# Kernel tuning notes

Hardware: AMD Instinct MI355X
Metric: run time of the kernel (lower is better)

## Reference

```python
import jax, jax.numpy as jnp
import numpy as np

INPUT_DIMS = 32
OUTPUT_DIMS = 1024
SEQ_LEN = 1024
BATCH = 64


def positional_encoding(max_len, d_model):
    pos = np.arange(max_len)[:, None].astype(np.float64)      # [L,1]
    i = np.arange(d_model)[None, :].astype(np.float64)        # [1,D]
    even_i = i - (i % 2)                                      # i for even, i-1 for odd
    angle = pos / np.power(10000.0, even_i / d_model)         # [L,D]
    pe = np.where(i % 2 == 0, np.sin(angle), np.cos(angle))
    return jnp.asarray(pe, dtype=jnp.float32)


def activation_quant(x):
    # per-token absmax int8 quant (BitNet b1.58)
    scale = 127.0 / jnp.clip(jnp.max(jnp.abs(x), axis=-1, keepdims=True), 1e-5, None)
    return jnp.clip(jnp.round(x * scale), -128, 127) / scale


def weight_quant(w):
    # per-tensor ternary quant via mean absmax
    scale = 1.0 / jnp.clip(jnp.mean(jnp.abs(w)), 1e-5, None)
    return jnp.clip(jnp.round(w * scale), -1, 1) / scale


def setup_inputs() -> dict:
    key = jax.random.key(0)
    k1, k2, k3 = jax.random.split(key, 3)
    x = jax.random.normal(k1, (BATCH, SEQ_LEN, INPUT_DIMS), dtype=jnp.float32)
    bound = 1.0 / np.sqrt(INPUT_DIMS)
    W = jax.random.uniform(k2, (OUTPUT_DIMS, INPUT_DIMS), minval=-bound, maxval=bound, dtype=jnp.float32)
    b = jax.random.uniform(k3, (OUTPUT_DIMS,), minval=-bound, maxval=bound, dtype=jnp.float32)
    return {"x": x, "W": W, "b": b}


def reference(x, W, b):
    # BitLinear with straight-through estimator
    x_eff = x + jax.lax.stop_gradient(activation_quant(x) - x)
    w_eff = W + jax.lax.stop_gradient(weight_quant(W) - W)
    emb = jnp.einsum('bsk,ok->bso', x_eff, w_eff) + b  # [B,S,O]
    pe = positional_encoding(SEQ_LEN, OUTPUT_DIMS)     # [L,O]
    return emb + pe[: emb.shape[-2]]
```

## Files before the change

### kernel.cpp

```cpp
#include <hip/hip_runtime.h>
#include <cstdint>
#include <cstddef>

#define BATCH   64
#define SEQLEN  1024
#define KDIM    32
#define ODIM    1024
#define NTOK    (BATCH * SEQLEN)

#define NWP 8
#define NQX 8192
#define NPE 1024

typedef __attribute__((ext_vector_type(8))) short bf16x8;
typedef __attribute__((ext_vector_type(4))) float f32x4;

__device__ __forceinline__ unsigned short f32_to_bf16_exact(float f) {
    union { float f; unsigned int u; } cv; cv.f = f;
    return (unsigned short)(cv.u >> 16);
}

__global__ __launch_bounds__(256) void prep_kernel(const float* __restrict__ x,
                                                   const float* __restrict__ W,
                                                   const float* __restrict__ bias,
                                                   float* __restrict__ partial,
                                                   unsigned short* __restrict__ xq,
                                                   float* __restrict__ rxs,
                                                   float* __restrict__ add) {
    const int blk = blockIdx.x;
    const int t   = threadIdx.x;

    if (blk < NWP) {
        __shared__ float red[256];
        const float4* W4 = reinterpret_cast<const float4*>(W) + (size_t)blk * 1024 + t * 4;
        float acc = 0.f;
        #pragma unroll
        for (int j = 0; j < 4; ++j) {
            float4 v = W4[j];
            acc += fabsf(v.x) + fabsf(v.y) + fabsf(v.z) + fabsf(v.w);
        }
        red[t] = acc;
        __syncthreads();
        for (int step = 128; step > 0; step >>= 1) {
            if (t < step) red[t] += red[t + step];
            __syncthreads();
        }
        if (t == 0) partial[blk] = red[0];
    } else if (blk < NWP + NQX) {
        const int idx = (blk - NWP) * 256 + t;
        float v = x[idx];
        float a = fabsf(v);
        #pragma unroll
        for (int off = 1; off < 32; off <<= 1)
            a = fmaxf(a, __shfl_xor(a, off, 32));
        float am = fmaxf(a, 1e-5f);
        float scale = 127.0f / am;
        xq[idx] = f32_to_bf16_exact(rintf(v * scale));
        if ((idx & 31) == 0) rxs[idx >> 5] = am * (1.0f / 127.0f);
    } else {
        const int g  = (blk - NWP - NQX) * 256 + t;
        const int oe = (g << 2) & (ODIM - 1);
        const int s  = g >> 8;
        const float C = -0.012976281620653759f;
        const float sf = (float)s;
        float a0 = sf * exp2f(C * (float)oe);
        float a1 = sf * exp2f(C * (float)(oe + 2));
        f32x4 bv = *reinterpret_cast<const f32x4*>(bias + oe);
        f32x4 r;
        r[0] = bv[0] + sinf(a0);
        r[1] = bv[1] + cosf(a0);
        r[2] = bv[2] + sinf(a1);
        r[3] = bv[3] + cosf(a1);
        *reinterpret_cast<f32x4*>(add + ((size_t)g << 2)) = r;
    }
}

__global__ __launch_bounds__(256) void bitgemm(
    const unsigned short* __restrict__ xq,
    const float*          __restrict__ rxs,
    const float*          __restrict__ W,
    const float*          __restrict__ partial,
    const float*          __restrict__ add,
    float* __restrict__ out)
{
    const int lane = threadIdx.x & 63;
    const int wid  = threadIdx.x >> 6;
    const int l15  = lane & 15;
    const int hi   = lane >> 4;

    const int lb   = (blockIdx.x & 7) * 256 + (blockIdx.x >> 3);
    const int oblk = lb & 31;
    const int sblk = lb >> 5;
    const int o0   = oblk * 32;
    const int s0   = sblk * 16;

    float tot = 0.f;
    #pragma unroll
    for (int p = 0; p < 8; ++p) tot += partial[p];
    const float rw = fmaxf(tot * (1.0f / 32768.0f), 1e-5f);
    const float sc = 1.0f / rw;

    bf16x8 afrag[2];
    #pragma unroll
    for (int f = 0; f < 2; ++f) {
        const float* wr = W + (size_t)(o0 + f * 16 + l15) * KDIM + hi * 8;
        float4 wa = *reinterpret_cast<const float4*>(wr);
        float4 wb = *reinterpret_cast<const float4*>(wr + 4);
        float e[8] = {wa.x, wa.y, wa.z, wa.w, wb.x, wb.y, wb.z, wb.w};
        union { bf16x8 v; unsigned short s[8]; } u;
        #pragma unroll
        for (int j = 0; j < 8; ++j)
            u.s[j] = f32_to_bf16_exact(fminf(fmaxf(rintf(e[j] * sc), -1.0f), 1.0f));
        afrag[f] = u.v;
    }

    f32x4 addf[2];
    #pragma unroll
    for (int f = 0; f < 2; ++f)
        addf[f] = *reinterpret_cast<const f32x4*>(
            add + (size_t)(s0 + l15) * ODIM + o0 + f * 16 + hi * 4);

    #pragma unroll 4
    for (int i = 0; i < 16; ++i) {
        const int b   = wid * 16 + i;
        const int tok = (b << 10) + s0 + l15;

        bf16x8 bfrag = *reinterpret_cast<const bf16x8*>(
            xq + ((size_t)tok << 5) + hi * 8);
        const float rxw = rxs[tok] * rw;

        float* op = out + ((size_t)tok << 10) + o0 + hi * 4;
        #pragma unroll
        for (int f = 0; f < 2; ++f) {
            f32x4 acc = (f32x4){0.f, 0.f, 0.f, 0.f};
            acc = __builtin_amdgcn_mfma_f32_16x16x32_bf16(afrag[f], bfrag, acc, 0, 0, 0);
            f32x4 r;
            #pragma unroll
            for (int j = 0; j < 4; ++j)
                r[j] = fmaf(acc[j], rxw, addf[f][j]);
            *reinterpret_cast<f32x4*>(op + f * 16) = r;
        }
    }
}

extern "C" void kernel_launch(void* const* d_in, const int* in_sizes, int n_in,
                              void* d_out, int out_size, void* d_ws, size_t ws_size,
                              hipStream_t stream) {
    const float* x = (const float*)d_in[0];
    const float* W = (const float*)d_in[1];
    const float* b = (const float*)d_in[2];
    float* out = (float*)d_out;

    char* wsb = (char*)d_ws;
    float*          partial = (float*)wsb;
    float*          rxs     = (float*)(wsb + 256);
    unsigned short* xq      = (unsigned short*)(wsb + (512u << 10));
    float*          add     = (float*)(wsb + (8u << 20));

    prep_kernel<<<NWP + NQX + NPE, 256, 0, stream>>>(x, W, b, partial, xq, rxs, add);
    bitgemm<<<2048, 256, 0, stream>>>(xq, rxs, W, partial, add, out);
}
```

Baseline: 66.46 us.

## Fuse positional-encoding table into GEMM and vectorise activation quantisation

Removes the precomputed bias+positional-encoding table from the prep kernel. Each GEMM thread now computes its own sin/cos values directly in registers, which drops a 4 MB workspace write and its later read. The activation quant pass now has each thread handle 8 contiguous elements with float4 loads and 16-byte stores. This cuts the prep grid from about 9K blocks to about 1K and shortens the shuffle reduction. The cost is extra transcendental math per GEMM thread, which is redundant across the 16 batch-stripe blocks.

```diff
diff --git a/kernel.cpp b/kernel.cpp
--- a/kernel.cpp
+++ b/kernel.cpp
@@ -9,8 +9,7 @@
 #define NTOK    (BATCH * SEQLEN)
 
 #define NWP 8
-#define NQX 8192
-#define NPE 1024
+#define NQX 1024
 
 typedef __attribute__((ext_vector_type(8))) short bf16x8;
 typedef __attribute__((ext_vector_type(4))) float f32x4;
@@ -22,11 +21,9 @@
 
 __global__ __launch_bounds__(256) void prep_kernel(const float* __restrict__ x,
                                                    const float* __restrict__ W,
-                                                   const float* __restrict__ bias,
                                                    float* __restrict__ partial,
                                                    unsigned short* __restrict__ xq,
-                                                   float* __restrict__ rxs,
-                                                   float* __restrict__ add) {
+                                                   float* __restrict__ rxs) {
     const int blk = blockIdx.x;
     const int t   = threadIdx.x;
 
@@ -46,32 +43,26 @@
             __syncthreads();
         }
         if (t == 0) partial[blk] = red[0];
-    } else if (blk < NWP + NQX) {
-        const int idx = (blk - NWP) * 256 + t;
-        float v = x[idx];
-        float a = fabsf(v);
+    } else {
+        const int g = (blk - NWP) * 256 + t;
+        const float* xg = x + ((size_t)g << 3);
+        float4 xa = *reinterpret_cast<const float4*>(xg);
+        float4 xb = *reinterpret_cast<const float4*>(xg + 4);
+        float a = fmaxf(fmaxf(fmaxf(fabsf(xa.x), fabsf(xa.y)),
+                              fmaxf(fabsf(xa.z), fabsf(xa.w))),
+                        fmaxf(fmaxf(fabsf(xb.x), fabsf(xb.y)),
+                              fmaxf(fabsf(xb.z), fabsf(xb.w))));
+        a = fmaxf(a, __shfl_xor(a, 1, 4));
+        a = fmaxf(a, __shfl_xor(a, 2, 4));
+        const float am = fmaxf(a, 1e-5f);
+        const float scale = 127.0f / am;
+        float e[8] = {xa.x, xa.y, xa.z, xa.w, xb.x, xb.y, xb.z, xb.w};
+        union { bf16x8 v; unsigned short s[8]; } u;
         #pragma unroll
-        for (int off = 1; off < 32; off <<= 1)
-            a = fmaxf(a, __shfl_xor(a, off, 32));
-        float am = fmaxf(a, 1e-5f);
-        float scale = 127.0f / am;
-        xq[idx] = f32_to_bf16_exact(rintf(v * scale));
-        if ((idx & 31) == 0) rxs[idx >> 5] = am * (1.0f / 127.0f);
-    } else {
-        const int g  = (blk - NWP - NQX) * 256 + t;
-        const int oe = (g << 2) & (ODIM - 1);
-        const int s  = g >> 8;
-        const float C = -0.012976281620653759f;
-        const float sf = (float)s;
-        float a0 = sf * exp2f(C * (float)oe);
-        float a1 = sf * exp2f(C * (float)(oe + 2));
-        f32x4 bv = *reinterpret_cast<const f32x4*>(bias + oe);
-        f32x4 r;
-        r[0] = bv[0] + sinf(a0);
-        r[1] = bv[1] + cosf(a0);
-        r[2] = bv[2] + sinf(a1);
-        r[3] = bv[3] + cosf(a1);
-        *reinterpret_cast<f32x4*>(add + ((size_t)g << 2)) = r;
+        for (int j = 0; j < 8; ++j)
+            u.s[j] = f32_to_bf16_exact(rintf(e[j] * scale));
+        *reinterpret_cast<bf16x8*>(xq + ((size_t)g << 3)) = u.v;
+        if ((g & 3) == 0) rxs[g >> 2] = am * (1.0f / 127.0f);
     }
 }
 
@@ -80,7 +71,7 @@
     const float*          __restrict__ rxs,
     const float*          __restrict__ W,
     const float*          __restrict__ partial,
-    const float*          __restrict__ add,
+    const float*          __restrict__ bias,
     float* __restrict__ out)
 {
     const int lane = threadIdx.x & 63;
@@ -114,11 +105,20 @@
         afrag[f] = u.v;
     }
 
+    const float C  = -0.012976281620653759f;
+    const float sf = (float)(s0 + l15);
     f32x4 addf[2];
     #pragma unroll
-    for (int f = 0; f < 2; ++f)
-        addf[f] = *reinterpret_cast<const f32x4*>(
-            add + (size_t)(s0 + l15) * ODIM + o0 + f * 16 + hi * 4);
+    for (int f = 0; f < 2; ++f) {
+        const int oe = o0 + f * 16 + hi * 4;
+        f32x4 bv = *reinterpret_cast<const f32x4*>(bias + oe);
+        float a0 = sf * exp2f(C * (float)oe);
+        float a1 = sf * exp2f(C * (float)(oe + 2));
+        addf[f][0] = bv[0] + sinf(a0);
+        addf[f][1] = bv[1] + cosf(a0);
+        addf[f][2] = bv[2] + sinf(a1);
+        addf[f][3] = bv[3] + cosf(a1);
+    }
 
     #pragma unroll 4
     for (int i = 0; i < 16; ++i) {
@@ -155,8 +155,7 @@
     float*          partial = (float*)wsb;
     float*          rxs     = (float*)(wsb + 256);
     unsigned short* xq      = (unsigned short*)(wsb + (512u << 10));
-    float*          add     = (float*)(wsb + (8u << 20));
 
-    prep_kernel<<<NWP + NQX + NPE, 256, 0, stream>>>(x, W, b, partial, xq, rxs, add);
-    bitgemm<<<2048, 256, 0, stream>>>(xq, rxs, W, partial, add, out);
+    prep_kernel<<<NWP + NQX, 256, 0, stream>>>(x, W, partial, xq, rxs);
+    bitgemm<<<2048, 256, 0, stream>>>(xq, rxs, W, partial, b, out);
 }
```

After: 62.18 us. 6.4% less time.
